# Kernel tuning notes

Hardware: AMD Instinct MI355X
Metric: run time of the kernel (lower is better)

The kernel has to match this reference:

```python
import jax, jax.numpy as jnp
import numpy as np

N, E, C, H, L, G, K, NC = 50000, 500000, 256, 128, 4, 64, 8, 2
EPS_MSG = 1e-7  # GENConv message eps
EPS_BN = 1e-5   # BatchNorm eps


def setup_inputs() -> dict:
    key = jax.random.key(0)
    ks = jax.random.split(key, 32)
    def nrm(k, shape, scale):
        return jax.random.normal(k, shape, dtype=jnp.float32) * scale
    sC = 1.0 / np.sqrt(C).astype(np.float32)
    sH = 1.0 / np.sqrt(H).astype(np.float32)
    s2H = 1.0 / np.sqrt(2 * H).astype(np.float32)
    return dict(
        x=nrm(ks[0], (N, C), 1.0),
        edge_index=jax.random.randint(ks[1], (2, E), 0, N, dtype=jnp.int32),
        edge_attr=jax.random.uniform(ks[2], (E, 1), dtype=jnp.float32),
        batch=jnp.sort(jax.random.randint(ks[3], (N,), 0, G, dtype=jnp.int32)),
        clinical=nrm(ks[4], (G, K), 1.0),
        lin_src_w=nrm(ks[5], (C, H), sC), lin_src_b=nrm(ks[6], (H,), 0.01),
        lin_dst_w=nrm(ks[7], (C, H), sC), lin_dst_b=nrm(ks[8], (H,), 0.01),
        edge_w=nrm(ks[9], (L, 1, H), 1.0), edge_b=nrm(ks[10], (L, H), 0.01),
        t=0.1 + 0.01 * jax.random.normal(ks[11], (L,), dtype=jnp.float32),
        mlp_w1=nrm(ks[12], (L, H, 2 * H), sH), mlp_b1=nrm(ks[13], (L, 2 * H), 0.01),
        mlp_bn_g=1.0 + nrm(ks[14], (L, 2 * H), 0.1), mlp_bn_b=nrm(ks[15], (L, 2 * H), 0.1),
        mlp_bn_m=nrm(ks[16], (L, 2 * H), 0.1),
        mlp_bn_v=1.0 + jax.random.uniform(ks[17], (L, 2 * H), dtype=jnp.float32),
        mlp_w2=nrm(ks[18], (L, 2 * H, H), s2H), mlp_b2=nrm(ks[19], (L, H), 0.01),
        norm_g=1.0 + nrm(ks[20], (L, H), 0.1), norm_b=nrm(ks[21], (L, H), 0.1),
        norm_m=nrm(ks[22], (L, H), 0.1),
        norm_v=1.0 + jax.random.uniform(ks[23], (L, H), dtype=jnp.float32),
        cls_w=nrm(ks[24], (H + K, NC), 1.0 / np.sqrt(H + K).astype(np.float32)),
        cls_b=nrm(ks[25], (NC,), 0.01),
    )


def _bn(h, g, b, m, v):
    # eval-mode BatchNorm with running stats
    return g * (h - m) * jax.lax.rsqrt(v + EPS_BN) + b


def reference(x, edge_index, edge_attr, batch, clinical,
              lin_src_w, lin_src_b, lin_dst_w, lin_dst_b,
              edge_w, edge_b, t,
              mlp_w1, mlp_b1, mlp_bn_g, mlp_bn_b, mlp_bn_m, mlp_bn_v,
              mlp_w2, mlp_b2, norm_g, norm_b, norm_m, norm_v,
              cls_w, cls_b):
    n = x.shape[0]
    g_count = clinical.shape[0]
    src, dst = edge_index[0], edge_index[1]
    n_layers = t.shape[0]

    def genconv(xs, xd, l):
        # xs: source features feeding messages [N,H]; xd: dst skip features [N,H]
        e = edge_attr @ edge_w[l] + edge_b[l]               # [E,H]
        msg = jax.nn.relu(xs[src] + e) + EPS_MSG            # [E,H]
        z = msg * t[l]
        zmax = jax.ops.segment_max(z, dst, num_segments=n)  # [N,H]
        zmax = jnp.where(jnp.isfinite(zmax), zmax, 0.0)
        ez = jnp.exp(z - zmax[dst])
        denom = jax.ops.segment_sum(ez, dst, num_segments=n)
        agg = jax.ops.segment_sum(msg * ez, dst, num_segments=n) / jnp.maximum(denom, 1e-16)
        out = agg + xd
        # internal MLP [H, 2H, H]: Linear -> BN -> ReLU -> Linear
        hmid = jax.nn.relu(_bn(out @ mlp_w1[l] + mlp_b1[l],
                               mlp_bn_g[l], mlp_bn_b[l], mlp_bn_m[l], mlp_bn_v[l]))
        return hmid @ mlp_w2[l] + mlp_b2[l]

    # layer 0: conv only (per DeepGCN.forward); lin_src / lin_dst project C -> H
    xs0 = x @ lin_src_w + lin_src_b
    xd0 = x @ lin_dst_w + lin_dst_b
    h = genconv(xs0, xd0, 0)

    # layers 1..L-1: res+ block (norm -> act -> conv, residual add); dropout = identity (eval)
    for l in range(1, n_layers):
        r = jax.nn.relu(_bn(h, norm_g[l], norm_b[l], norm_m[l], norm_v[l]))
        h = h + genconv(r, r, l)

    # final norm/act from layer 0
    h = jax.nn.relu(_bn(h, norm_g[0], norm_b[0], norm_m[0], norm_v[0]))

    # global mean pool over graphs
    cnt = jax.ops.segment_sum(jnp.ones((n,), h.dtype), batch, num_segments=g_count)
    pooled = jax.ops.segment_sum(h, batch, num_segments=g_count) / jnp.maximum(cnt, 1.0)[:, None]

    z = jnp.concatenate([pooled, clinical], axis=1)
    return z @ cls_w + cls_b  # [G, num_classes]; squeeze is a no-op for G>1, NC=2
```

## Files before the change

kernel.cpp:

```cpp
#include <hip/hip_runtime.h>
#include <math.h>

#define Nn 50000
#define MPAD 50048
#define Ee 500000
#define Cc 256
#define Hh 128
#define Ll 4
#define Gg 64
#define Kk 8
#define NCc 2

#define NB 196

typedef __attribute__((ext_vector_type(8))) short short8;
typedef __attribute__((ext_vector_type(4))) float f32x4;
typedef __attribute__((ext_vector_type(2))) float f32x2;

__device__ __forceinline__ unsigned short f2bf(float f) {
    union { float f; unsigned int u; } v;
    v.f = f;
    unsigned int u = v.u;
    return (unsigned short)((u + 0x7FFFu + ((u >> 16) & 1u)) >> 16);
}
__device__ __forceinline__ float bf2f(unsigned short s) {
    union { float f; unsigned int u; } v;
    v.u = ((unsigned int)s) << 16;
    return v.f;
}
__device__ __forceinline__ float bf2f_lo(unsigned int u) {
    union { float f; unsigned int u; } v;
    v.u = u << 16;
    return v.f;
}
__device__ __forceinline__ float bf2f_hi(unsigned int u) {
    union { float f; unsigned int u; } v;
    v.u = u & 0xffff0000u;
    return v.f;
}


__global__ void hist_kernel(const int* __restrict__ dst, int* __restrict__ deg) {
    int e = blockIdx.x * 256 + threadIdx.x;
    if (e < Ee) atomicAdd(&deg[dst[e]], 1);
}

__global__ __launch_bounds__(256) void bsum_kernel(const int* __restrict__ deg,
                                                   int* __restrict__ bsum) {
    __shared__ int ws[4];
    int t = threadIdx.x;
    int i = blockIdx.x * 256 + t;
    int v = (i < Nn) ? deg[i] : 0;
#pragma unroll
    for (int o = 32; o; o >>= 1) v += __shfl_down(v, o, 64);
    if ((t & 63) == 0) ws[t >> 6] = v;
    __syncthreads();
    if (t == 0) bsum[blockIdx.x] = ws[0] + ws[1] + ws[2] + ws[3];
}

__global__ __launch_bounds__(256) void bscan_kernel(const int* __restrict__ bsum,
                                                    int* __restrict__ boff,
                                                    int* __restrict__ off) {
    __shared__ int sc[256];
    int t = threadIdx.x;
    int v = (t < NB) ? bsum[t] : 0;
    sc[t] = v;
    __syncthreads();
    for (int o = 1; o < 256; o <<= 1) {
        int u = (t >= o) ? sc[t - o] : 0;
        __syncthreads();
        sc[t] += u;
        __syncthreads();
    }
    if (t < NB) boff[t] = sc[t] - v;
    if (t == NB - 1) off[Nn] = sc[t];
}

__global__ __launch_bounds__(256) void offsets_kernel(const int* __restrict__ deg,
                                                      const int* __restrict__ boff,
                                                      int* __restrict__ off,
                                                      int* __restrict__ pos) {
    __shared__ int sc[256];
    int t = threadIdx.x;
    int i = blockIdx.x * 256 + t;
    int v = (i < Nn) ? deg[i] : 0;
    sc[t] = v;
    __syncthreads();
    for (int o = 1; o < 256; o <<= 1) {
        int u = (t >= o) ? sc[t - o] : 0;
        __syncthreads();
        sc[t] += u;
        __syncthreads();
    }
    int excl = sc[t] - v + boff[blockIdx.x];
    if (i < Nn) {
        off[i] = excl;
        pos[i] = excl;
    }
}

__global__ void scatter_kernel(const int* __restrict__ src, const int* __restrict__ dst,
                               const float* __restrict__ attr, int* __restrict__ pos,
                               int2* __restrict__ sedge) {
    int e = blockIdx.x * 256 + threadIdx.x;
    if (e < Ee) {
        int d = dst[e];
        int p = atomicAdd(&pos[d], 1);
        sedge[p] = make_int2(src[e], __float_as_int(attr[e]));
    }
}


__global__ void wconv_kernel(const float* __restrict__ lin_src_w,
                             const float* __restrict__ lin_dst_w,
                             const float* __restrict__ mlp_w1,
                             const float* __restrict__ mlp_w2,
                             unsigned short* __restrict__ wt) {
    int idx = blockIdx.x * 256 + threadIdx.x;
    if (idx >= 327680) return;
    float val;
    if (idx < 65536) {
        int n = idx >> 8, k = idx & 255;
        val = (n < 128) ? lin_src_w[k * 128 + n] : lin_dst_w[k * 128 + (n - 128)];
    } else if (idx < 196608) {
        int r = idx - 65536;
        int l = r >> 15, e = r & 32767;
        int n = e >> 7, k = e & 127;
        val = mlp_w1[(size_t)l * 32768 + k * 256 + n];
    } else {
        int r = idx - 196608;
        int l = r >> 15, e = r & 32767;
        int n = e >> 8, k = e & 255;
        val = mlp_w2[(size_t)l * 32768 + k * 128 + n];
    }
    wt[idx] = f2bf(val);
}


__global__ __launch_bounds__(256) void xconv_kernel(const float* __restrict__ x,
                                                    unsigned short* __restrict__ xbf) {
    int idx = blockIdx.x * 256 + threadIdx.x;
    if (idx >= (Nn * Cc) / 8) return;
    const float4* p = (const float4*)(x) + (size_t)idx * 2;
    float4 v0 = p[0], v1 = p[1];
    unsigned short t[8];
    t[0] = f2bf(v0.x); t[1] = f2bf(v0.y); t[2] = f2bf(v0.z); t[3] = f2bf(v0.w);
    t[4] = f2bf(v1.x); t[5] = f2bf(v1.y); t[6] = f2bf(v1.z); t[7] = f2bf(v1.w);
    *(short8*)(xbf + (size_t)idx * 8) = *(short8*)t;
}


#define BM 128
#define BK 32

#define GLOAD16(gp, lp)                                                                       \
    __builtin_amdgcn_global_load_lds(                                                         \
        (const __attribute__((address_space(1))) unsigned int*)(gp),                          \
        (__attribute__((address_space(3))) unsigned int*)(lp), 16, 0, 0)

template <int BNt>
__global__ __launch_bounds__(256) void gemm_kernel(
    const unsigned short* __restrict__ A, const unsigned short* __restrict__ Bt,
    const float* __restrict__ bias, const float* __restrict__ bias2,
    const float* __restrict__ bn_g, const float* __restrict__ bn_b,
    const float* __restrict__ bn_m, const float* __restrict__ bn_v,
    const float* __restrict__ pn_g, const float* __restrict__ pn_b,
    const float* __restrict__ pn_m, const float* __restrict__ pn_v,
    float* __restrict__ CoutF, unsigned short* __restrict__ CoutB,
    unsigned short* __restrict__ Rbuf, int N, int K, int mode) {
    constexpr int WC = BNt / 64;
    constexpr int WR = 4 / WC;
    constexpr int MT = BM / (WR * 16);
    constexpr int BCH = (BNt * BK) / 2048;

    __shared__ __align__(16) unsigned short As[2][BM * BK];
    __shared__ __align__(16) unsigned short Bs[2][BNt * BK];

    int tid = threadIdx.x;
    int wave = tid >> 6, lane = tid & 63;
    int wr = wave / WC, wc = wave % WC;
    int lrow = lane & 15, quad = lane >> 4;
    int m0 = blockIdx.y * BM, n0 = blockIdx.x * BNt;

    const unsigned short* ag0 = A + (size_t)(m0 + (tid >> 2)) * K + (tid & 3) * 8;
    const unsigned short* ag1 = A + (size_t)(m0 + 64 + (tid >> 2)) * K + (tid & 3) * 8;
    const unsigned short* bg0 = Bt + (size_t)(n0 + (tid >> 2)) * K + (tid & 3) * 8;
    const unsigned short* bg1 =
        (BCH == 2) ? (Bt + (size_t)(n0 + 64 + (tid >> 2)) * K + (tid & 3) * 8) : nullptr;

    f32x4 acc[MT][4];
#pragma unroll
    for (int i = 0; i < MT; i++)
#pragma unroll
        for (int j = 0; j < 4; j++) acc[i][j] = (f32x4){0.f, 0.f, 0.f, 0.f};

    auto stage = [&](int buf, int koff) {
        GLOAD16(ag0 + koff, &As[buf][wave * 512]);
        GLOAD16(ag1 + koff, &As[buf][2048 + wave * 512]);
        GLOAD16(bg0 + koff, &Bs[buf][wave * 512]);
        if constexpr (BCH == 2) GLOAD16(bg1 + koff, &Bs[buf][2048 + wave * 512]);
    };

    int ntiles = K / BK;
    stage(0, 0);
    __syncthreads();
    for (int t = 0; t < ntiles; ++t) {
        if (t + 1 < ntiles) stage((t + 1) & 1, (t + 1) * BK);
        int cur = t & 1;
        short8 af[MT], bfr[4];
#pragma unroll
        for (int mt = 0; mt < MT; mt++)
            af[mt] = *(const short8*)&As[cur][(wr * (MT * 16) + mt * 16 + lrow) * BK + quad * 8];
#pragma unroll
        for (int nf = 0; nf < 4; nf++)
            bfr[nf] = *(const short8*)&Bs[cur][(wc * 64 + nf * 16 + lrow) * BK + quad * 8];
#pragma unroll
        for (int mt = 0; mt < MT; mt++)
#pragma unroll
            for (int nf = 0; nf < 4; nf++)
                acc[mt][nf] = __builtin_amdgcn_mfma_f32_16x16x32_bf16(af[mt], bfr[nf],
                                                                     acc[mt][nf], 0, 0, 0);
        __syncthreads();
    }

#pragma unroll
    for (int nf = 0; nf < 4; nf++) {
        int gc = n0 + wc * 64 + nf * 16 + lrow;
        float bs = (bias2 && gc >= 128) ? bias2[gc - 128] : (bias ? bias[gc] : 0.f);
        float g = 1.f, bb = 0.f, mm = 0.f, inv = 1.f;
        if (mode == 1) {
            g = bn_g[gc];
            bb = bn_b[gc];
            mm = bn_m[gc];
            inv = rsqrtf(bn_v[gc] + 1e-5f);
        }
        float pg = 0.f, pb = 0.f, pm = 0.f, pinv = 0.f;
        if (mode >= 2 && pn_g) {
            pg = pn_g[gc];
            pb = pn_b[gc];
            pm = pn_m[gc];
            pinv = rsqrtf(pn_v[gc] + 1e-5f);
        }
#pragma unroll
        for (int mt = 0; mt < MT; mt++) {
#pragma unroll
            for (int r = 0; r < 4; r++) {
                int gr = m0 + wr * (MT * 16) + mt * 16 + quad * 4 + r;
                size_t idx = (size_t)gr * N + gc;
                float v = acc[mt][nf][r] + bs;
                if (mode == 0) {
                    CoutB[idx] = f2bf(v);
                } else if (mode == 1) {
                    v = fmaxf(g * (v - mm) * inv + bb, 0.f);
                    CoutB[idx] = f2bf(v);
                } else {
                    if (mode == 2) v += CoutF[idx];
                    CoutF[idx] = v;
                    if (pn_g)
                        Rbuf[idx] = f2bf(fmaxf(pg * (v - pm) * pinv + pb, 0.f));
                }
            }
        }
    }
}


template <int XSS>
__global__ __launch_bounds__(256) void agg_kernel(
    const unsigned short* __restrict__ xs,
    const unsigned short* __restrict__ xd, int xds,
    const int2* __restrict__ sedge, const int* __restrict__ off,
    const float* __restrict__ ew, const float* __restrict__ eb,
    const float* __restrict__ tptr, unsigned short* __restrict__ outb) {
    int wave = threadIdx.x >> 6;
    int lane = threadIdx.x & 63;
    int d = blockIdx.x * 4 + wave;
    int s0 = off[d], s1 = off[d + 1];
    int f0 = lane * 2;
    f32x2 wv = *(const f32x2*)(ew + f0);
    f32x2 bv = *(const f32x2*)(eb + f0);
    float c = tptr[0] * 1.44269504088896f;
    const f32x2 zz = {0.f, 0.f};
    const f32x2 ee = {1e-7f, 1e-7f};
    f32x2 den = {0.f, 0.f}, num = {0.f, 0.f};

#define EDGE2(u, av)                                                      \
    {                                                                     \
        f32x2 xv = {bf2f_lo(u), bf2f_hi(u)};                              \
        f32x2 m = __builtin_elementwise_max(xv + bv + (av)*wv, zz) + ee;  \
        f32x2 e;                                                          \
        e.x = __builtin_amdgcn_exp2f(m.x * c);                            \
        e.y = __builtin_amdgcn_exp2f(m.y * c);                            \
        den += e;                                                         \
        num += m * e;                                                     \
    }

    int j = s0;
    for (; j + 3 < s1; j += 4) {
        int2 p0 = sedge[j], p1 = sedge[j + 1], p2 = sedge[j + 2], p3 = sedge[j + 3];
        unsigned int u0 = *(const unsigned int*)(xs + (size_t)p0.x * XSS + f0);
        unsigned int u1 = *(const unsigned int*)(xs + (size_t)p1.x * XSS + f0);
        unsigned int u2 = *(const unsigned int*)(xs + (size_t)p2.x * XSS + f0);
        unsigned int u3 = *(const unsigned int*)(xs + (size_t)p3.x * XSS + f0);
        EDGE2(u0, __int_as_float(p0.y))
        EDGE2(u1, __int_as_float(p1.y))
        EDGE2(u2, __int_as_float(p2.y))
        EDGE2(u3, __int_as_float(p3.y))
    }
    for (; j < s1; j++) {
        int2 p = sedge[j];
        unsigned int u = *(const unsigned int*)(xs + (size_t)p.x * XSS + f0);
        EDGE2(u, __int_as_float(p.y))
    }
#undef EDGE2
    float a0 = (s1 > s0) ? (num.x / fmaxf(den.x, 1e-16f)) : 0.f;
    float a1 = (s1 > s0) ? (num.y / fmaxf(den.y, 1e-16f)) : 0.f;
    unsigned int ud = *(const unsigned int*)(xd + (size_t)d * xds + f0);
    unsigned int lo = f2bf(a0 + bf2f_lo(ud));
    unsigned int hi = f2bf(a1 + bf2f_hi(ud));
    *(unsigned int*)(outb + (size_t)d * Hh + f0) = lo | (hi << 16);
}


#define PCHUNK 100

__global__ __launch_bounds__(128) void pool_kernel(
    const float* __restrict__ h, const int* __restrict__ batch,
    const float* __restrict__ g, const float* __restrict__ b,
    const float* __restrict__ m, const float* __restrict__ v,
    float* __restrict__ pooled, float* __restrict__ cnt) {
    int hh = threadIdx.x;
    int i0 = blockIdx.x * PCHUNK;
    int i1 = min(i0 + PCHUNK, Nn);
    if (i0 >= Nn) return;
    float gg = g[hh], bb = b[hh], mm = m[hh], inv = rsqrtf(v[hh] + 1e-5f);
    int cur = batch[i0];
    float sum = 0.f, c = 0.f;
    for (int i = i0; i < i1; i++) {
        int gid = batch[i];
        float val = fmaxf(gg * (h[(size_t)i * Hh + hh] - mm) * inv + bb, 0.f);
        if (gid != cur) {
            atomicAdd(&pooled[(size_t)cur * Hh + hh], sum);
            if (hh == 0) atomicAdd(&cnt[cur], c);
            cur = gid;
            sum = 0.f;
            c = 0.f;
        }
        sum += val;
        c += 1.f;
    }
    atomicAdd(&pooled[(size_t)cur * Hh + hh], sum);
    if (hh == 0) atomicAdd(&cnt[cur], c);
}


__global__ __launch_bounds__(128) void cls_kernel(const float* __restrict__ pooled,
                                                  const float* __restrict__ cnt,
                                                  const float* __restrict__ clinical,
                                                  const float* __restrict__ w,
                                                  const float* __restrict__ bias,
                                                  float* __restrict__ out) {
    int t = threadIdx.x;
    int g = t >> 1, c = t & 1;
    float inv = 1.f / fmaxf(cnt[g], 1.f);
    float s = bias[c];
    for (int j = 0; j < Hh; j++) s += pooled[g * Hh + j] * inv * w[j * NCc + c];
    for (int k = 0; k < Kk; k++) s += clinical[g * Kk + k] * w[(Hh + k) * NCc + c];
    out[g * NCc + c] = s;
}


extern "C" void kernel_launch(void* const* d_in, const int* in_sizes, int n_in,
                              void* d_out, int out_size, void* d_ws, size_t ws_size,
                              hipStream_t stream) {
    const float* x = (const float*)d_in[0];
    const int* eidx = (const int*)d_in[1];
    const float* eattr = (const float*)d_in[2];
    const int* batch = (const int*)d_in[3];
    const float* clinical = (const float*)d_in[4];
    const float* lin_src_w = (const float*)d_in[5];
    const float* lin_src_b = (const float*)d_in[6];
    const float* lin_dst_w = (const float*)d_in[7];
    const float* lin_dst_b = (const float*)d_in[8];
    const float* edge_w = (const float*)d_in[9];
    const float* edge_b = (const float*)d_in[10];
    const float* tt = (const float*)d_in[11];
    const float* mlp_w1 = (const float*)d_in[12];
    const float* mlp_b1 = (const float*)d_in[13];
    const float* bn_g = (const float*)d_in[14];
    const float* bn_b = (const float*)d_in[15];
    const float* bn_m = (const float*)d_in[16];
    const float* bn_v = (const float*)d_in[17];
    const float* mlp_w2 = (const float*)d_in[18];
    const float* mlp_b2 = (const float*)d_in[19];
    const float* norm_g = (const float*)d_in[20];
    const float* norm_b = (const float*)d_in[21];
    const float* norm_m = (const float*)d_in[22];
    const float* norm_v = (const float*)d_in[23];
    const float* cls_w = (const float*)d_in[24];
    const float* cls_b = (const float*)d_in[25];
    float* out = (float*)d_out;

    const int* src = eidx;
    const int* dst = eidx + Ee;

    char* ws = (char*)d_ws;
    size_t off_b = 0;
    auto alloc = [&](size_t bytes) -> void* {
        void* p = ws + off_b;
        off_b += (bytes + 255) & ~(size_t)255;
        return p;
    };
    unsigned short* xsd = (unsigned short*)alloc((size_t)MPAD * 256 * 2);
    unsigned short* rbuf = (unsigned short*)alloc((size_t)MPAD * Hh * 2);
    unsigned short* aggout = (unsigned short*)alloc((size_t)MPAD * Hh * 2);
    unsigned short* hmid = (unsigned short*)alloc((size_t)MPAD * 2 * Hh * 2);
    float* hbuf = (float*)alloc((size_t)MPAD * Hh * 4);
    int* deg = (int*)alloc((Nn + 1) * 4);
    int* offp = (int*)alloc((Nn + 1) * 4);
    int* pos = (int*)alloc((size_t)Nn * 4);
    int* bsum = (int*)alloc(NB * 4);
    int* boff = (int*)alloc(NB * 4);
    int2* sedge = (int2*)alloc((size_t)Ee * 8);
    float* pooled = (float*)alloc((size_t)Gg * Hh * 4);
    float* cntb = (float*)alloc(Gg * 4);
    unsigned short* wt = (unsigned short*)alloc((size_t)327680 * 2);
    unsigned short* xbf = hmid;

    hipMemsetAsync(deg, 0, (Nn + 1) * 4, stream);
    hipMemsetAsync(pooled, 0, (size_t)Gg * Hh * 4, stream);
    hipMemsetAsync(cntb, 0, Gg * 4, stream);

    hist_kernel<<<(Ee + 255) / 256, 256, 0, stream>>>(dst, deg);
    bsum_kernel<<<NB, 256, 0, stream>>>(deg, bsum);
    bscan_kernel<<<1, 256, 0, stream>>>(bsum, boff, offp);
    offsets_kernel<<<NB, 256, 0, stream>>>(deg, boff, offp, pos);
    scatter_kernel<<<(Ee + 255) / 256, 256, 0, stream>>>(src, dst, eattr, pos, sedge);
    wconv_kernel<<<1280, 256, 0, stream>>>(lin_src_w, lin_dst_w, mlp_w1, mlp_w2, wt);
    xconv_kernel<<<(Nn * Cc / 8 + 255) / 256, 256, 0, stream>>>(x, xbf);

    const unsigned short* wt_proj = wt;
    const unsigned short* wt_w1 = wt + 65536;
    const unsigned short* wt_w2 = wt + 196608;

    dim3 gproj(256 / 128, MPAD / BM);
    gemm_kernel<128><<<gproj, 256, 0, stream>>>(xbf, wt_proj, lin_src_b, lin_dst_b,
                                                nullptr, nullptr, nullptr, nullptr,
                                                nullptr, nullptr, nullptr, nullptr,
                                                nullptr, xsd, nullptr, 256, Cc, 0);

    for (int l = 0; l < Ll; l++) {
        if (l == 0) {
            agg_kernel<256><<<Nn / 4, 256, 0, stream>>>(xsd, xsd + 128, 256, sedge, offp,
                                                        edge_w + l * Hh, edge_b + l * Hh,
                                                        tt + l, aggout);
        } else {
            agg_kernel<128><<<Nn / 4, 256, 0, stream>>>(rbuf, rbuf, Hh, sedge, offp,
                                                        edge_w + l * Hh, edge_b + l * Hh,
                                                        tt + l, aggout);
        }
        dim3 g1((2 * Hh) / 128, MPAD / BM);
        gemm_kernel<128><<<g1, 256, 0, stream>>>(aggout, wt_w1 + (size_t)l * 32768,
                                                 mlp_b1 + l * 2 * Hh, nullptr,
                                                 bn_g + l * 2 * Hh, bn_b + l * 2 * Hh,
                                                 bn_m + l * 2 * Hh, bn_v + l * 2 * Hh,
                                                 nullptr, nullptr, nullptr, nullptr,
                                                 nullptr, hmid, nullptr, 2 * Hh, Hh, 1);
        const float* png = (l < Ll - 1) ? (norm_g + (l + 1) * Hh) : nullptr;
        const float* pnb = (l < Ll - 1) ? (norm_b + (l + 1) * Hh) : nullptr;
        const float* pnm = (l < Ll - 1) ? (norm_m + (l + 1) * Hh) : nullptr;
        const float* pnv = (l < Ll - 1) ? (norm_v + (l + 1) * Hh) : nullptr;
        dim3 g2(Hh / 64, MPAD / BM);
        gemm_kernel<64><<<g2, 256, 0, stream>>>(hmid, wt_w2 + (size_t)l * 32768,
                                                mlp_b2 + l * Hh, nullptr,
                                                nullptr, nullptr, nullptr, nullptr,
                                                png, pnb, pnm, pnv,
                                                hbuf, nullptr, rbuf, Hh, 2 * Hh,
                                                (l == 0) ? 3 : 2);
    }

    pool_kernel<<<(Nn + PCHUNK - 1) / PCHUNK, 128, 0, stream>>>(hbuf, batch, norm_g, norm_b,
                                                                norm_m, norm_v, pooled, cntb);
    cls_kernel<<<1, 128, 0, stream>>>(pooled, cntb, clinical, cls_w, cls_b, out);
}
```

Before: 603.6 us.

## Fuse per-layer MLP GEMMs into one kernel and restage projection epilogue

Replaces the two per-layer MLP GEMM launches with one fused kernel. It computes Linear→BN→ReLU into a shared-memory hidden tile, runs the second Linear from that tile, and applies the residual add and next-layer norm in a vectorized epilogue. This removes the global round trip of the 2H-wide bf16 intermediate and one launch per layer. The projection GEMM becomes a specialized kernel with a 3-stage LDS pipeline using explicit vmcnt waits and coalesced stores staged through LDS. Costs: the fused kernel recomputes nothing but uses a 64-row tile and about 74 KB of LDS, which may lower occupancy, and xbf now gets its own buffer.

Result: faster. 509.8 us (-15.5%).

```diff
diff --git a/kernel.cpp b/kernel.cpp
--- a/kernel.cpp
+++ b/kernel.cpp
@@ -149,117 +149,239 @@
     *(short8*)(xbf + (size_t)idx * 8) = *(short8*)t;
 }
 
-
-#define BM 128
-#define BK 32
-
 #define GLOAD16(gp, lp)                                                                       \
     __builtin_amdgcn_global_load_lds(                                                         \
         (const __attribute__((address_space(1))) unsigned int*)(gp),                          \
         (__attribute__((address_space(3))) unsigned int*)(lp), 16, 0, 0)
 
-template <int BNt>
-__global__ __launch_bounds__(256) void gemm_kernel(
+
+__global__ __launch_bounds__(256) void proj_kernel(
     const unsigned short* __restrict__ A, const unsigned short* __restrict__ Bt,
     const float* __restrict__ bias, const float* __restrict__ bias2,
-    const float* __restrict__ bn_g, const float* __restrict__ bn_b,
-    const float* __restrict__ bn_m, const float* __restrict__ bn_v,
-    const float* __restrict__ pn_g, const float* __restrict__ pn_b,
-    const float* __restrict__ pn_m, const float* __restrict__ pn_v,
-    float* __restrict__ CoutF, unsigned short* __restrict__ CoutB,
-    unsigned short* __restrict__ Rbuf, int N, int K, int mode) {
-    constexpr int WC = BNt / 64;
-    constexpr int WR = 4 / WC;
-    constexpr int MT = BM / (WR * 16);
-    constexpr int BCH = (BNt * BK) / 2048;
-
-    __shared__ __align__(16) unsigned short As[2][BM * BK];
-    __shared__ __align__(16) unsigned short Bs[2][BNt * BK];
-
+    unsigned short* __restrict__ Cout) {
+    __shared__ __align__(16) unsigned short SH[24576];
     int tid = threadIdx.x;
     int wave = tid >> 6, lane = tid & 63;
-    int wr = wave / WC, wc = wave % WC;
+    int wr = wave >> 1, wc = wave & 1;
     int lrow = lane & 15, quad = lane >> 4;
-    int m0 = blockIdx.y * BM, n0 = blockIdx.x * BNt;
+    int m0 = blockIdx.y * 128, n0 = blockIdx.x * 128;
+    const int K = 256;
 
     const unsigned short* ag0 = A + (size_t)(m0 + (tid >> 2)) * K + (tid & 3) * 8;
     const unsigned short* ag1 = A + (size_t)(m0 + 64 + (tid >> 2)) * K + (tid & 3) * 8;
     const unsigned short* bg0 = Bt + (size_t)(n0 + (tid >> 2)) * K + (tid & 3) * 8;
-    const unsigned short* bg1 =
-        (BCH == 2) ? (Bt + (size_t)(n0 + 64 + (tid >> 2)) * K + (tid & 3) * 8) : nullptr;
-
-    f32x4 acc[MT][4];
-#pragma unroll
-    for (int i = 0; i < MT; i++)
+    const unsigned short* bg1 = Bt + (size_t)(n0 + 64 + (tid >> 2)) * K + (tid & 3) * 8;
+
+    f32x4 acc[4][4];
+#pragma unroll
+    for (int i = 0; i < 4; i++)
 #pragma unroll
         for (int j = 0; j < 4; j++) acc[i][j] = (f32x4){0.f, 0.f, 0.f, 0.f};
 
     auto stage = [&](int buf, int koff) {
-        GLOAD16(ag0 + koff, &As[buf][wave * 512]);
-        GLOAD16(ag1 + koff, &As[buf][2048 + wave * 512]);
-        GLOAD16(bg0 + koff, &Bs[buf][wave * 512]);
-        if constexpr (BCH == 2) GLOAD16(bg1 + koff, &Bs[buf][2048 + wave * 512]);
+        GLOAD16(ag0 + koff, SH + buf * 4096 + wave * 512);
+        GLOAD16(ag1 + koff, SH + buf * 4096 + 2048 + wave * 512);
+        GLOAD16(bg0 + koff, SH + 12288 + buf * 4096 + wave * 512);
+        GLOAD16(bg1 + koff, SH + 12288 + buf * 4096 + 2048 + wave * 512);
     };
 
-    int ntiles = K / BK;
+    const int ntiles = 8;
     stage(0, 0);
-    __syncthreads();
+    stage(1, 32);
     for (int t = 0; t < ntiles; ++t) {
-        if (t + 1 < ntiles) stage((t + 1) & 1, (t + 1) * BK);
-        int cur = t & 1;
-        short8 af[MT], bfr[4];
-#pragma unroll
-        for (int mt = 0; mt < MT; mt++)
-            af[mt] = *(const short8*)&As[cur][(wr * (MT * 16) + mt * 16 + lrow) * BK + quad * 8];
+        if (t + 1 < ntiles) {
+            asm volatile("s_waitcnt vmcnt(4)\n\ts_barrier" ::: "memory");
+        } else {
+            asm volatile("s_waitcnt vmcnt(0)\n\ts_barrier" ::: "memory");
+        }
+        if (t + 2 < ntiles) stage((t + 2) % 3, (t + 2) * 32);
+        int cur = t % 3;
+        const unsigned short* As = SH + cur * 4096;
+        const unsigned short* Bs = SH + 12288 + cur * 4096;
+        short8 af[4], bfr[4];
+#pragma unroll
+        for (int mt = 0; mt < 4; mt++)
+            af[mt] = *(const short8*)&As[(wr * 64 + mt * 16 + lrow) * 32 + quad * 8];
 #pragma unroll
         for (int nf = 0; nf < 4; nf++)
-            bfr[nf] = *(const short8*)&Bs[cur][(wc * 64 + nf * 16 + lrow) * BK + quad * 8];
-#pragma unroll
-        for (int mt = 0; mt < MT; mt++)
+            bfr[nf] = *(const short8*)&Bs[(wc * 64 + nf * 16 + lrow) * 32 + quad * 8];
+#pragma unroll
+        for (int mt = 0; mt < 4; mt++)
 #pragma unroll
             for (int nf = 0; nf < 4; nf++)
                 acc[mt][nf] = __builtin_amdgcn_mfma_f32_16x16x32_bf16(af[mt], bfr[nf],
                                                                      acc[mt][nf], 0, 0, 0);
-        __syncthreads();
-    }
-
+    }
+
+    __syncthreads();
+    unsigned short* Cl = SH;
 #pragma unroll
     for (int nf = 0; nf < 4; nf++) {
         int gc = n0 + wc * 64 + nf * 16 + lrow;
-        float bs = (bias2 && gc >= 128) ? bias2[gc - 128] : (bias ? bias[gc] : 0.f);
-        float g = 1.f, bb = 0.f, mm = 0.f, inv = 1.f;
-        if (mode == 1) {
-            g = bn_g[gc];
-            bb = bn_b[gc];
-            mm = bn_m[gc];
-            inv = rsqrtf(bn_v[gc] + 1e-5f);
-        }
-        float pg = 0.f, pb = 0.f, pm = 0.f, pinv = 0.f;
-        if (mode >= 2 && pn_g) {
-            pg = pn_g[gc];
-            pb = pn_b[gc];
-            pm = pn_m[gc];
-            pinv = rsqrtf(pn_v[gc] + 1e-5f);
-        }
-#pragma unroll
-        for (int mt = 0; mt < MT; mt++) {
+        float bs = (gc >= 128) ? bias2[gc - 128] : bias[gc];
+        int col = wc * 64 + nf * 16 + lrow;
+#pragma unroll
+        for (int mt = 0; mt < 4; mt++)
+#pragma unroll
+            for (int r = 0; r < 4; r++)
+                Cl[(wr * 64 + mt * 16 + quad * 4 + r) * 128 + col] = f2bf(acc[mt][nf][r] + bs);
+    }
+    __syncthreads();
+#pragma unroll
+    for (int p = 0; p < 8; p++) {
+        int vid = p * 256 + tid;
+        int row = vid >> 4, cg = (vid & 15) * 8;
+        short8 v = *(const short8*)&Cl[row * 128 + cg];
+        *(short8*)(Cout + (size_t)(m0 + row) * 256 + n0 + cg) = v;
+    }
+}
+
+
+__global__ __launch_bounds__(256) void mlp_kernel(
+    const unsigned short* __restrict__ A,
+    const unsigned short* __restrict__ W1,
+    const unsigned short* __restrict__ W2,
+    const float* __restrict__ b1, const float* __restrict__ bn_g,
+    const float* __restrict__ bn_b, const float* __restrict__ bn_m,
+    const float* __restrict__ bn_v, const float* __restrict__ b2,
+    const float* __restrict__ pn_g, const float* __restrict__ pn_b,
+    const float* __restrict__ pn_m, const float* __restrict__ pn_v,
+    float* __restrict__ hbuf, unsigned short* __restrict__ rbuf, int rmw) {
+    __shared__ __align__(16) unsigned short S[20480];
+    __shared__ __align__(16) unsigned short Hm[64 * 264];
+
+    int tid = threadIdx.x;
+    int wave = tid >> 6, lane = tid & 63;
+    int lrow = lane & 15, quad = lane >> 4;
+    int m0 = blockIdx.x * 64;
+
+    const unsigned short* ag = A + (size_t)(m0 + (tid >> 2)) * 128 + (tid & 3) * 8;
+    const unsigned short* bg = W1 + (size_t)(tid >> 2) * 128 + (tid & 3) * 8;
+
+    f32x4 acc1[4][4];
+#pragma unroll
+    for (int i = 0; i < 4; i++)
+#pragma unroll
+        for (int j = 0; j < 4; j++) acc1[i][j] = (f32x4){0.f, 0.f, 0.f, 0.f};
+
+    auto stage1 = [&](int buf, int k0) {
+        GLOAD16(ag + k0, S + buf * 2048 + wave * 512);
+#pragma unroll
+        for (int c = 0; c < 4; c++)
+            GLOAD16(bg + (size_t)c * 64 * 128 + k0,
+                    S + 4096 + buf * 8192 + c * 2048 + wave * 512);
+    };
+
+    stage1(0, 0);
+    __syncthreads();
+    for (int t = 0; t < 4; ++t) {
+        if (t + 1 < 4) stage1((t + 1) & 1, (t + 1) * 32);
+        int cur = t & 1;
+        const unsigned short* A1s = S + cur * 2048;
+        const unsigned short* B1s = S + 4096 + cur * 8192;
+        short8 af[4], bfr[4];
+#pragma unroll
+        for (int mt = 0; mt < 4; mt++)
+            af[mt] = *(const short8*)&A1s[(mt * 16 + lrow) * 32 + quad * 8];
+#pragma unroll
+        for (int nf = 0; nf < 4; nf++)
+            bfr[nf] = *(const short8*)&B1s[(wave * 64 + nf * 16 + lrow) * 32 + quad * 8];
+#pragma unroll
+        for (int mt = 0; mt < 4; mt++)
+#pragma unroll
+            for (int nf = 0; nf < 4; nf++)
+                acc1[mt][nf] = __builtin_amdgcn_mfma_f32_16x16x32_bf16(af[mt], bfr[nf],
+                                                                      acc1[mt][nf], 0, 0, 0);
+        __syncthreads();
+    }
+
+#pragma unroll
+    for (int nf = 0; nf < 4; nf++) {
+        int gc = wave * 64 + nf * 16 + lrow;
+        float bs = b1[gc];
+        float g = bn_g[gc], bb = bn_b[gc], mm = bn_m[gc];
+        float inv = rsqrtf(bn_v[gc] + 1e-5f);
+#pragma unroll
+        for (int mt = 0; mt < 4; mt++)
 #pragma unroll
             for (int r = 0; r < 4; r++) {
-                int gr = m0 + wr * (MT * 16) + mt * 16 + quad * 4 + r;
-                size_t idx = (size_t)gr * N + gc;
-                float v = acc[mt][nf][r] + bs;
-                if (mode == 0) {
-                    CoutB[idx] = f2bf(v);
-                } else if (mode == 1) {
-                    v = fmaxf(g * (v - mm) * inv + bb, 0.f);
-                    CoutB[idx] = f2bf(v);
-                } else {
-                    if (mode == 2) v += CoutF[idx];
-                    CoutF[idx] = v;
-                    if (pn_g)
-                        Rbuf[idx] = f2bf(fmaxf(pg * (v - pm) * pinv + pb, 0.f));
-                }
+                float v = acc1[mt][nf][r] + bs;
+                v = fmaxf(g * (v - mm) * inv + bb, 0.f);
+                Hm[(mt * 16 + quad * 4 + r) * 264 + gc] = f2bf(v);
             }
+    }
+    __syncthreads();
+
+    const unsigned short* b2g0 = W2 + (size_t)(tid >> 2) * 256 + (tid & 3) * 8;
+    const unsigned short* b2g1 = W2 + (size_t)(64 + (tid >> 2)) * 256 + (tid & 3) * 8;
+
+    f32x4 acc2[4][2];
+#pragma unroll
+    for (int i = 0; i < 4; i++)
+#pragma unroll
+        for (int j = 0; j < 2; j++) acc2[i][j] = (f32x4){0.f, 0.f, 0.f, 0.f};
+
+    auto stage2 = [&](int buf, int k0) {
+        GLOAD16(b2g0 + k0, S + buf * 4096 + wave * 512);
+        GLOAD16(b2g1 + k0, S + buf * 4096 + 2048 + wave * 512);
+    };
+
+    stage2(0, 0);
+    __syncthreads();
+    for (int t = 0; t < 8; ++t) {
+        if (t + 1 < 8) stage2((t + 1) & 1, (t + 1) * 32);
+        int cur = t & 1;
+        const unsigned short* B2s = S + cur * 4096;
+        short8 af[4], bfr[2];
+#pragma unroll
+        for (int mt = 0; mt < 4; mt++)
+            af[mt] = *(const short8*)&Hm[(mt * 16 + lrow) * 264 + t * 32 + quad * 8];
+#pragma unroll
+        for (int nf = 0; nf < 2; nf++)
+            bfr[nf] = *(const short8*)&B2s[(wave * 32 + nf * 16 + lrow) * 32 + quad * 8];
+#pragma unroll
+        for (int mt = 0; mt < 4; mt++)
+#pragma unroll
+            for (int nf = 0; nf < 2; nf++)
+                acc2[mt][nf] = __builtin_amdgcn_mfma_f32_16x16x32_bf16(af[mt], bfr[nf],
+                                                                      acc2[mt][nf], 0, 0, 0);
+        __syncthreads();
+    }
+
+    float* C2 = (float*)S;
+#pragma unroll
+    for (int nf = 0; nf < 2; nf++) {
+        int gc = wave * 32 + nf * 16 + lrow;
+        float bs = b2[gc];
+#pragma unroll
+        for (int mt = 0; mt < 4; mt++)
+#pragma unroll
+            for (int r = 0; r < 4; r++)
+                C2[(mt * 16 + quad * 4 + r) * 128 + gc] = acc2[mt][nf][r] + bs;
+    }
+    __syncthreads();
+#pragma unroll
+    for (int p = 0; p < 8; p++) {
+        int vid = p * 256 + tid;
+        int row = vid >> 5, c4 = (vid & 31) * 4;
+        f32x4 v = *(const f32x4*)&C2[row * 128 + c4];
+        float* hp = hbuf + (size_t)(m0 + row) * 128 + c4;
+        if (rmw) v += *(const f32x4*)hp;
+        *(f32x4*)hp = v;
+        if (pn_g) {
+            f32x4 pg = *(const f32x4*)&pn_g[c4];
+            f32x4 pb = *(const f32x4*)&pn_b[c4];
+            f32x4 pm = *(const f32x4*)&pn_m[c4];
+            f32x4 pv = *(const f32x4*)&pn_v[c4];
+            unsigned int w0, w1;
+            float r0 = fmaxf(pg[0] * (v[0] - pm[0]) * rsqrtf(pv[0] + 1e-5f) + pb[0], 0.f);
+            float r1 = fmaxf(pg[1] * (v[1] - pm[1]) * rsqrtf(pv[1] + 1e-5f) + pb[1], 0.f);
+            float r2 = fmaxf(pg[2] * (v[2] - pm[2]) * rsqrtf(pv[2] + 1e-5f) + pb[2], 0.f);
+            float r3 = fmaxf(pg[3] * (v[3] - pm[3]) * rsqrtf(pv[3] + 1e-5f) + pb[3], 0.f);
+            w0 = (unsigned int)f2bf(r0) | ((unsigned int)f2bf(r1) << 16);
+            w1 = (unsigned int)f2bf(r2) | ((unsigned int)f2bf(r3) << 16);
+            uint2 pk = make_uint2(w0, w1);
+            *(uint2*)(rbuf + (size_t)(m0 + row) * 128 + c4) = pk;
         }
     }
 }
@@ -414,7 +536,7 @@
     unsigned short* xsd = (unsigned short*)alloc((size_t)MPAD * 256 * 2);
     unsigned short* rbuf = (unsigned short*)alloc((size_t)MPAD * Hh * 2);
     unsigned short* aggout = (unsigned short*)alloc((size_t)MPAD * Hh * 2);
-    unsigned short* hmid = (unsigned short*)alloc((size_t)MPAD * 2 * Hh * 2);
+    unsigned short* xbf = (unsigned short*)alloc((size_t)MPAD * 256 * 2);
     float* hbuf = (float*)alloc((size_t)MPAD * Hh * 4);
     int* deg = (int*)alloc((Nn + 1) * 4);
     int* offp = (int*)alloc((Nn + 1) * 4);
@@ -425,7 +547,6 @@
     float* pooled = (float*)alloc((size_t)Gg * Hh * 4);
     float* cntb = (float*)alloc(Gg * 4);
     unsigned short* wt = (unsigned short*)alloc((size_t)327680 * 2);
-    unsigned short* xbf = hmid;
 
     hipMemsetAsync(deg, 0, (Nn + 1) * 4, stream);
     hipMemsetAsync(pooled, 0, (size_t)Gg * Hh * 4, stream);
@@ -443,11 +564,8 @@
     const unsigned short* wt_w1 = wt + 65536;
     const unsigned short* wt_w2 = wt + 196608;
 
-    dim3 gproj(256 / 128, MPAD / BM);
-    gemm_kernel<128><<<gproj, 256, 0, stream>>>(xbf, wt_proj, lin_src_b, lin_dst_b,
-                                                nullptr, nullptr, nullptr, nullptr,
-                                                nullptr, nullptr, nullptr, nullptr,
-                                                nullptr, xsd, nullptr, 256, Cc, 0);
+    dim3 gproj(2, MPAD / 128);
+    proj_kernel<<<gproj, 256, 0, stream>>>(xbf, wt_proj, lin_src_b, lin_dst_b, xsd);
 
     for (int l = 0; l < Ll; l++) {
         if (l == 0) {
@@ -459,24 +577,15 @@
                                                         edge_w + l * Hh, edge_b + l * Hh,
                                                         tt + l, aggout);
         }
-        dim3 g1((2 * Hh) / 128, MPAD / BM);
-        gemm_kernel<128><<<g1, 256, 0, stream>>>(aggout, wt_w1 + (size_t)l * 32768,
-                                                 mlp_b1 + l * 2 * Hh, nullptr,
-                                                 bn_g + l * 2 * Hh, bn_b + l * 2 * Hh,
-                                                 bn_m + l * 2 * Hh, bn_v + l * 2 * Hh,
-                                                 nullptr, nullptr, nullptr, nullptr,
-                                                 nullptr, hmid, nullptr, 2 * Hh, Hh, 1);
         const float* png = (l < Ll - 1) ? (norm_g + (l + 1) * Hh) : nullptr;
         const float* pnb = (l < Ll - 1) ? (norm_b + (l + 1) * Hh) : nullptr;
         const float* pnm = (l < Ll - 1) ? (norm_m + (l + 1) * Hh) : nullptr;
         const float* pnv = (l < Ll - 1) ? (norm_v + (l + 1) * Hh) : nullptr;
-        dim3 g2(Hh / 64, MPAD / BM);
-        gemm_kernel<64><<<g2, 256, 0, stream>>>(hmid, wt_w2 + (size_t)l * 32768,
-                                                mlp_b2 + l * Hh, nullptr,
-                                                nullptr, nullptr, nullptr, nullptr,
-                                                png, pnb, pnm, pnv,
-                                                hbuf, nullptr, rbuf, Hh, 2 * Hh,
-                                                (l == 0) ? 3 : 2);
+        mlp_kernel<<<MPAD / 64, 256, 0, stream>>>(
+            aggout, wt_w1 + (size_t)l * 32768, wt_w2 + (size_t)l * 32768,
+            mlp_b1 + l * 2 * Hh, bn_g + l * 2 * Hh, bn_b + l * 2 * Hh,
+            bn_m + l * 2 * Hh, bn_v + l * 2 * Hh, mlp_b2 + l * Hh,
+            png, pnb, pnm, pnv, hbuf, rbuf, (l == 0) ? 0 : 1);
     }
 
     pool_kernel<<<(Nn + PCHUNK - 1) / PCHUNK, 128, 0, stream>>>(hbuf, batch, norm_g, norm_b,
```
